# Kernel optimization log

Hardware: AMD Instinct MI355X
Metric: run time of the kernel (lower is better)

The kernel has to match this reference:

```python
import jax, jax.numpy as jnp
import numpy as np


def setup_inputs() -> dict:
    key = jax.random.key(0)
    ks = jax.random.split(key, 6)
    B, C, S, E = 8, 16, 512, 256
    wscale = (2.0 / (E + E)) ** 0.5  # xavier_normal for [E, E] fan_in=fan_out=E
    return {
        "query": jax.random.normal(ks[0], (B, C, S, E), dtype=jnp.float32),
        "key": jax.random.normal(ks[1], (B, C, S, E), dtype=jnp.float32),
        "value": jax.random.normal(ks[2], (B, C, S, E), dtype=jnp.float32),
        "q_proj_weight": jax.random.normal(ks[3], (C, E, E), dtype=jnp.float32) * wscale,
        "k_proj_weight": jax.random.normal(ks[4], (C, E, E), dtype=jnp.float32) * wscale,
        "v_proj_weight": jax.random.normal(ks[5], (C, E, E), dtype=jnp.float32) * wscale,
        "q_proj_bias": jnp.zeros((C, 1, E), dtype=jnp.float32),
        "k_proj_bias": jnp.zeros((C, 1, E), dtype=jnp.float32),
        "v_proj_bias": jnp.zeros((C, 1, E), dtype=jnp.float32),
    }


def reference(query, key, value, q_proj_weight, k_proj_weight, v_proj_weight,
              q_proj_bias, k_proj_bias, v_proj_bias):
    E = query.shape[-1]
    # Per-cycle projection + bias + ReLU.  b=batch, c=cycle, s/t=seq, e/f=embed
    q = jax.nn.relu(jnp.einsum("bcse,cef->bcsf", query, q_proj_weight) + q_proj_bias)
    k = jax.nn.relu(jnp.einsum("bcse,cef->bcsf", key, k_proj_weight) + k_proj_bias)
    v = jax.nn.relu(jnp.einsum("bcse,cef->bcsf", value, v_proj_weight) + v_proj_bias)
    q = q * (float(E) ** -0.5)
    attn = jax.nn.softmax(jnp.einsum("bcse,bcte->bcst", q, k), axis=-1)
    out = jnp.einsum("bcst,bcte->bcse", attn, v)
    return out
```

## Files before the change

### kernel.cpp

```cpp
#include <hip/hip_runtime.h>

constexpr int BATCH = 8;
constexpr int CYC   = 16;
constexpr int SEQ   = 512;
constexpr int EMB   = 256;

typedef __attribute__((ext_vector_type(8))) short bf16x8;
typedef __attribute__((ext_vector_type(4))) float f32x4;

__device__ __forceinline__ unsigned short f2bf(float x) {
    unsigned int u = __float_as_uint(x);
    u += 0x7fffu + ((u >> 16) & 1u);
    return (unsigned short)(u >> 16);
}
__device__ __forceinline__ unsigned int pk2(float lo, float hi) {
    return (unsigned int)f2bf(lo) | ((unsigned int)f2bf(hi) << 16);
}

__device__ __forceinline__ f32x4 mfma16(bf16x8 a, bf16x8 b, f32x4 c) {
    return __builtin_amdgcn_mfma_f32_16x16x32_bf16(a, b, c, 0, 0, 0);
}

__device__ __forceinline__ void gll16(const unsigned short* g, unsigned short* l) {
    __builtin_amdgcn_global_load_lds(
        (const __attribute__((address_space(1))) void*)g,
        (__attribute__((address_space(3))) void*)l, 16, 0, 0);
}

__global__ __launch_bounds__(256) void wt_kernel(const float* __restrict__ W,
                                                 unsigned short* __restrict__ Wt) {
    __shared__ float tile[64][65];
    const int c  = blockIdx.z;
    const int e0 = blockIdx.x * 64;
    const int f0 = blockIdx.y * 64;
    const float* Wc = W + (size_t)c * EMB * EMB;
    unsigned short* Wtc = Wt + (size_t)c * EMB * EMB;
    const int t = threadIdx.x;
    {
        const int er = t >> 4;
        const int fc = (t & 15) * 4;
        for (int i = 0; i < 4; ++i) {
            const float4 v = *(const float4*)(Wc + (size_t)(e0 + er + i * 16) * EMB + f0 + fc);
            tile[er + i * 16][fc + 0] = v.x;
            tile[er + i * 16][fc + 1] = v.y;
            tile[er + i * 16][fc + 2] = v.z;
            tile[er + i * 16][fc + 3] = v.w;
        }
    }
    __syncthreads();
    {
        const int fr = t >> 4;
        const int ec = (t & 15) * 4;
        for (int i = 0; i < 4; ++i) {
            const int f = fr + i * 16;
            ushort4 o;
            o.x = f2bf(tile[ec + 0][f]);
            o.y = f2bf(tile[ec + 1][f]);
            o.z = f2bf(tile[ec + 2][f]);
            o.w = f2bf(tile[ec + 3][f]);
            *(ushort4*)(Wtc + (size_t)(f0 + f) * EMB + e0 + ec) = o;
        }
    }
}

__global__ __launch_bounds__(256) void proj_kernel(
    const float* __restrict__ X, const unsigned short* __restrict__ Wt,
    const float* __restrict__ bias, unsigned short* __restrict__ Y,
    const float scale, const int transposeOut)
{
    __shared__ unsigned short smem[10752];
    unsigned short* As = smem;
    unsigned short* Bs = smem + 2560;
    const int bc = blockIdx.x;
    const int c  = bc & (CYC - 1);
    const int m0 = blockIdx.y * 64;
    const float* Xb = X + (size_t)bc * SEQ * EMB;
    const unsigned short* Wc = Wt + (size_t)c * EMB * EMB;
    const float* bb = bias + (size_t)c * EMB;
    unsigned short* Yb = Y + (size_t)bc * SEQ * EMB;

    const int tid  = threadIdx.x;
    const int lane = tid & 63, w = tid >> 6;
    const int ln   = lane & 15, quad = lane >> 4;
    const int wu   = __builtin_amdgcn_readfirstlane(w);

    const int arow = tid >> 2;
    const int acol = (tid & 3) * 8;
    const int brow = lane >> 2;
    const int gch  = (lane & 3) ^ ((lane >> 3) & 3);
    const int bslot = quad ^ ((ln >> 1) & 3);

    f32x4 acc[4][4];
    for (int i = 0; i < 4; ++i)
        for (int j = 0; j < 4; ++j) acc[i][j] = (f32x4){0.f, 0.f, 0.f, 0.f};

    for (int kk = 0; kk < 8; ++kk) {
        const int k0 = kk * 32;
        const float* ax = Xb + (size_t)(m0 + arow) * EMB + k0 + acol;
        const float4 a0 = *(const float4*)ax;
        const float4 a1 = *(const float4*)(ax + 4);
        int4 pk;
        pk.x = pk2(a0.x, a0.y); pk.y = pk2(a0.z, a0.w);
        pk.z = pk2(a1.x, a1.y); pk.w = pk2(a1.z, a1.w);
        *(int4*)&As[arow * 40 + acol] = pk;
        for (int j = 0; j < 4; ++j) {
            const int r = wu * 64 + j * 16 + brow;
            gll16(Wc + (size_t)r * EMB + k0 + gch * 8,
                  Bs + (size_t)(wu * 64 + j * 16) * 32);
        }
        __syncthreads();
        bf16x8 af[4], bfv[4];
        for (int i = 0; i < 4; ++i)
            af[i] = *(const bf16x8*)&As[(i * 16 + ln) * 40 + quad * 8];
        for (int j = 0; j < 4; ++j)
            bfv[j] = *(const bf16x8*)&Bs[(w * 64 + j * 16 + ln) * 32 + bslot * 8];
        for (int i = 0; i < 4; ++i)
            for (int j = 0; j < 4; ++j)
                acc[i][j] = mfma16(af[i], bfv[j], acc[i][j]);
        __syncthreads();
    }

    float bvj[4];
    for (int j = 0; j < 4; ++j) bvj[j] = bb[w * 64 + j * 16 + ln];

    if (!transposeOut) {
        unsigned short* ep = smem + w * 1152;
        for (int i = 0; i < 4; ++i) {
            for (int j = 0; j < 4; ++j)
                for (int r = 0; r < 4; ++r)
                    ep[(quad * 4 + r) * 72 + j * 16 + ln] =
                        f2bf(fmaxf(acc[i][j][r] + bvj[j], 0.f) * scale);
            __syncthreads();
            for (int h = 0; h < 2; ++h) {
                const int cid = lane + h * 64;
                const int row = cid >> 3, ch = cid & 7;
                *(bf16x8*)&Yb[(size_t)(m0 + i * 16 + row) * EMB + w * 64 + ch * 8] =
                    *(const bf16x8*)&ep[row * 72 + ch * 8];
            }
            __syncthreads();
        }
    } else {
        for (int j = 0; j < 4; ++j) {
            const int fg = w * 64 + j * 16 + ln;
            for (int i = 0; i < 4; ++i) {
                const int mb = m0 + i * 16 + quad * 4;
                ushort4 u;
                u.x = f2bf(fmaxf(acc[i][j][0] + bvj[j], 0.f) * scale);
                u.y = f2bf(fmaxf(acc[i][j][1] + bvj[j], 0.f) * scale);
                u.z = f2bf(fmaxf(acc[i][j][2] + bvj[j], 0.f) * scale);
                u.w = f2bf(fmaxf(acc[i][j][3] + bvj[j], 0.f) * scale);
                *(ushort4*)&Yb[(size_t)fg * SEQ + mb] = u;
            }
        }
    }
}

__global__ __launch_bounds__(256) void attn_kernel(
    const unsigned short* __restrict__ Qp, const unsigned short* __restrict__ Kp,
    const unsigned short* __restrict__ Vt, float* __restrict__ Out)
{
    __shared__ unsigned short Ks[32][264];
    __shared__ unsigned short Vs[256][40];
    __shared__ unsigned short Ps[64][40];
    const int bc = blockIdx.x;
    const int qt = blockIdx.y;
    const unsigned short* Qb = Qp + (size_t)bc * SEQ * EMB;
    const unsigned short* Kb = Kp + (size_t)bc * SEQ * EMB;
    const unsigned short* Vb = Vt + (size_t)bc * SEQ * EMB;
    float* Ob = Out + (size_t)bc * SEQ * EMB;

    const int tid  = threadIdx.x;
    const int lane = tid & 63, w = tid >> 6;
    const int ln   = lane & 15, quad = lane >> 4;

    bf16x8 qf[8];
    const int qrow = qt * 64 + w * 16 + ln;
    for (int ke = 0; ke < 8; ++ke)
        qf[ke] = *(const bf16x8*)(Qb + (size_t)qrow * EMB + ke * 32 + quad * 8);

    f32x4 of[16];
    for (int n = 0; n < 16; ++n) of[n] = (f32x4){0.f, 0.f, 0.f, 0.f};
    float lsum[4] = {0.f, 0.f, 0.f, 0.f};

    for (int tt = 0; tt < 16; ++tt) {
        const int t0 = tt * 32;
        for (int i = 0; i < 4; ++i) {
            const int idx = tid + i * 256;
            const int r = idx >> 5, c8 = (idx & 31) * 8;
            *(bf16x8*)&Ks[r][c8] = *(const bf16x8*)(Kb + (size_t)(t0 + r) * EMB + c8);
        }
        for (int i = 0; i < 4; ++i) {
            const int idx = tid + i * 256;
            const int e = idx >> 2, c8 = (idx & 3) * 8;
            *(bf16x8*)&Vs[e][c8] = *(const bf16x8*)(Vb + (size_t)e * SEQ + t0 + c8);
        }
        __syncthreads();

        f32x4 sf0 = (f32x4){0.f,0.f,0.f,0.f}, sf1 = (f32x4){0.f,0.f,0.f,0.f};
        for (int ke = 0; ke < 8; ++ke) {
            bf16x8 b0 = *(const bf16x8*)&Ks[ln][ke * 32 + quad * 8];
            bf16x8 b1 = *(const bf16x8*)&Ks[16 + ln][ke * 32 + quad * 8];
            sf0 = mfma16(qf[ke], b0, sf0);
            sf1 = mfma16(qf[ke], b1, sf1);
        }

        float p0[4], p1[4];
        for (int r = 0; r < 4; ++r) {
            p0[r] = __expf(sf0[r]);
            p1[r] = __expf(sf1[r]);
            lsum[r] += p0[r] + p1[r];
        }
        for (int r = 0; r < 4; ++r) {
            Ps[w * 16 + quad * 4 + r][ln]      = f2bf(p0[r]);
            Ps[w * 16 + quad * 4 + r][16 + ln] = f2bf(p1[r]);
        }
        __syncthreads();

        bf16x8 af = *(const bf16x8*)&Ps[w * 16 + ln][quad * 8];
        for (int n = 0; n < 16; ++n) {
            bf16x8 bv = *(const bf16x8*)&Vs[n * 16 + ln][quad * 8];
            of[n] = mfma16(af, bv, of[n]);
        }
        __syncthreads();
    }

    for (int off = 1; off < 16; off <<= 1)
        for (int r = 0; r < 4; ++r)
            lsum[r] += __shfl_xor(lsum[r], off, 64);
    float inv[4];
    for (int r = 0; r < 4; ++r) inv[r] = 1.0f / lsum[r];
    const int mbase = qt * 64 + w * 16 + quad * 4;
    for (int n = 0; n < 16; ++n)
        for (int r = 0; r < 4; ++r)
            Ob[(size_t)(mbase + r) * EMB + n * 16 + ln] = of[n][r] * inv[r];
}

extern "C" void kernel_launch(void* const* d_in, const int* in_sizes, int n_in,
                              void* d_out, int out_size, void* d_ws, size_t ws_size,
                              hipStream_t stream) {
    const float* query = (const float*)d_in[0];
    const float* key_  = (const float*)d_in[1];
    const float* value = (const float*)d_in[2];
    const float* wq = (const float*)d_in[3];
    const float* wk = (const float*)d_in[4];
    const float* wv = (const float*)d_in[5];
    const float* bq = (const float*)d_in[6];
    const float* bk = (const float*)d_in[7];
    const float* bv = (const float*)d_in[8];
    float* out = (float*)d_out;

    char* ws = (char*)d_ws;
    const size_t wsz = (size_t)CYC * EMB * EMB * sizeof(unsigned short);
    const size_t psz = (size_t)BATCH * CYC * SEQ * EMB * sizeof(unsigned short);
    unsigned short* Wtq = (unsigned short*)(ws);
    unsigned short* Wtk = (unsigned short*)(ws + wsz);
    unsigned short* Wtv = (unsigned short*)(ws + 2 * wsz);
    unsigned short* Qp  = (unsigned short*)(ws + 3 * wsz);
    unsigned short* Kp  = (unsigned short*)(ws + 3 * wsz + psz);
    unsigned short* Vtp = (unsigned short*)(ws + 3 * wsz + 2 * psz);

    const dim3 tb(256);
    wt_kernel<<<dim3(4, 4, CYC), tb, 0, stream>>>(wq, Wtq);
    wt_kernel<<<dim3(4, 4, CYC), tb, 0, stream>>>(wk, Wtk);
    wt_kernel<<<dim3(4, 4, CYC), tb, 0, stream>>>(wv, Wtv);

    const dim3 pg(BATCH * CYC, SEQ / 64);
    proj_kernel<<<pg, tb, 0, stream>>>(query, Wtq, bq, Qp, 0.0625f, 0);
    proj_kernel<<<pg, tb, 0, stream>>>(key_,  Wtk, bk, Kp, 1.0f, 0);
    proj_kernel<<<pg, tb, 0, stream>>>(value, Wtv, bv, Vtp, 1.0f, 1);

    attn_kernel<<<dim3(BATCH * CYC, SEQ / 64), tb, 0, stream>>>(Qp, Kp, Vtp, out);
}
```

Baseline: 352.4 us.

## Merge launches, pre-swizzle weights, double-buffer proj and attention K tiles

Combines the three weight-transpose launches and the three projection launches into one launch each, selecting Q/K/V by blockIdx.z. The weight-transpose kernel now writes the transposed weights in a k-chunked, pre-swizzled layout, so the projection kernel can fetch contiguous 16-byte chunks with global_load_lds into double-buffered LDS, overlapping the next tile's loads with the current MFMAs. The attention kernel double-buffers K tiles in XOR-swizzled LDS and loads V fragments straight from global into registers instead of staging them through LDS. Occupancy hints are added to the launch bounds. The aim is to cut launch overhead and load latency, at the cost of more LDS and registers per block and uncoalesced direct V loads.

```diff
diff --git a/kernel.cpp b/kernel.cpp
--- a/kernel.cpp
+++ b/kernel.cpp
@@ -16,64 +16,76 @@
 __device__ __forceinline__ unsigned int pk2(float lo, float hi) {
     return (unsigned int)f2bf(lo) | ((unsigned int)f2bf(hi) << 16);
 }
-
 __device__ __forceinline__ f32x4 mfma16(bf16x8 a, bf16x8 b, f32x4 c) {
     return __builtin_amdgcn_mfma_f32_16x16x32_bf16(a, b, c, 0, 0, 0);
 }
-
 __device__ __forceinline__ void gll16(const unsigned short* g, unsigned short* l) {
     __builtin_amdgcn_global_load_lds(
         (const __attribute__((address_space(1))) void*)g,
         (__attribute__((address_space(3))) void*)l, 16, 0, 0);
 }
 
-__global__ __launch_bounds__(256) void wt_kernel(const float* __restrict__ W,
-                                                 unsigned short* __restrict__ Wt) {
-    __shared__ float tile[64][65];
-    const int c  = blockIdx.z;
-    const int e0 = blockIdx.x * 64;
+__global__ __launch_bounds__(256) void wt_kernel(
+    const float* __restrict__ Wq, const float* __restrict__ Wk, const float* __restrict__ Wv,
+    unsigned short* __restrict__ Oq, unsigned short* __restrict__ Ok, unsigned short* __restrict__ Ov)
+{
+    __shared__ float tile[32][65];
+    const int kk = blockIdx.x;
     const int f0 = blockIdx.y * 64;
+    const int z  = blockIdx.z;
+    const int which = z >> 4, c = z & 15;
+    const float* W = which == 0 ? Wq : (which == 1 ? Wk : Wv);
+    unsigned short* O = which == 0 ? Oq : (which == 1 ? Ok : Ov);
     const float* Wc = W + (size_t)c * EMB * EMB;
-    unsigned short* Wtc = Wt + (size_t)c * EMB * EMB;
+    unsigned short* Oc = O + (size_t)c * EMB * EMB;
     const int t = threadIdx.x;
     {
-        const int er = t >> 4;
-        const int fc = (t & 15) * 4;
-        for (int i = 0; i < 4; ++i) {
-            const float4 v = *(const float4*)(Wc + (size_t)(e0 + er + i * 16) * EMB + f0 + fc);
-            tile[er + i * 16][fc + 0] = v.x;
-            tile[er + i * 16][fc + 1] = v.y;
-            tile[er + i * 16][fc + 2] = v.z;
-            tile[er + i * 16][fc + 3] = v.w;
-        }
+        const int er = t >> 3, fc = (t & 7) * 8;
+        const float4 v0 = *(const float4*)(Wc + (size_t)(kk * 32 + er) * EMB + f0 + fc);
+        const float4 v1 = *(const float4*)(Wc + (size_t)(kk * 32 + er) * EMB + f0 + fc + 4);
+        tile[er][fc + 0] = v0.x; tile[er][fc + 1] = v0.y;
+        tile[er][fc + 2] = v0.z; tile[er][fc + 3] = v0.w;
+        tile[er][fc + 4] = v1.x; tile[er][fc + 5] = v1.y;
+        tile[er][fc + 6] = v1.z; tile[er][fc + 7] = v1.w;
     }
     __syncthreads();
     {
-        const int fr = t >> 4;
-        const int ec = (t & 15) * 4;
-        for (int i = 0; i < 4; ++i) {
-            const int f = fr + i * 16;
-            ushort4 o;
-            o.x = f2bf(tile[ec + 0][f]);
-            o.y = f2bf(tile[ec + 1][f]);
-            o.z = f2bf(tile[ec + 2][f]);
-            o.w = f2bf(tile[ec + 3][f]);
-            *(ushort4*)(Wtc + (size_t)(f0 + f) * EMB + e0 + ec) = o;
-        }
-    }
-}
-
-__global__ __launch_bounds__(256) void proj_kernel(
-    const float* __restrict__ X, const unsigned short* __restrict__ Wt,
-    const float* __restrict__ bias, unsigned short* __restrict__ Y,
-    const float scale, const int transposeOut)
+        const int fl = t >> 2, s = t & 3;
+        const int f  = f0 + fl;
+        const int e0 = (s ^ ((f >> 1) & 3)) * 8;
+        ushort4 o0, o1;
+        o0.x = f2bf(tile[e0 + 0][fl]); o0.y = f2bf(tile[e0 + 1][fl]);
+        o0.z = f2bf(tile[e0 + 2][fl]); o0.w = f2bf(tile[e0 + 3][fl]);
+        o1.x = f2bf(tile[e0 + 4][fl]); o1.y = f2bf(tile[e0 + 5][fl]);
+        o1.z = f2bf(tile[e0 + 6][fl]); o1.w = f2bf(tile[e0 + 7][fl]);
+        unsigned short* dst = Oc + (size_t)kk * 8192 + (size_t)f * 32 + s * 8;
+        *(ushort4*)dst       = o0;
+        *(ushort4*)(dst + 4) = o1;
+    }
+}
+
+__global__ __launch_bounds__(256, 3) void proj_kernel(
+    const float* __restrict__ Xq, const float* __restrict__ Xk, const float* __restrict__ Xv,
+    const unsigned short* __restrict__ Wq, const unsigned short* __restrict__ Wk,
+    const unsigned short* __restrict__ Wv,
+    const float* __restrict__ bq, const float* __restrict__ bk, const float* __restrict__ bv,
+    unsigned short* __restrict__ Yq, unsigned short* __restrict__ Yk, unsigned short* __restrict__ Yv)
 {
-    __shared__ unsigned short smem[10752];
-    unsigned short* As = smem;
-    unsigned short* Bs = smem + 2560;
+    __shared__ unsigned short smem[21504];
+    unsigned short* Asb[2] = { smem,        smem + 2560 };
+    unsigned short* Bsb[2] = { smem + 5120, smem + 13312 };
+
     const int bc = blockIdx.x;
+    const int m0 = blockIdx.y * 64;
+    const int which = blockIdx.z;
     const int c  = bc & (CYC - 1);
-    const int m0 = blockIdx.y * 64;
+    const float* X = which == 0 ? Xq : (which == 1 ? Xk : Xv);
+    const unsigned short* Wt = which == 0 ? Wq : (which == 1 ? Wk : Wv);
+    const float* bias = which == 0 ? bq : (which == 1 ? bk : bv);
+    unsigned short* Y = which == 0 ? Yq : (which == 1 ? Yk : Yv);
+    const float scale = which == 0 ? 0.0625f : 1.0f;
+    const int transposeOut = (which == 2);
+
     const float* Xb = X + (size_t)bc * SEQ * EMB;
     const unsigned short* Wc = Wt + (size_t)c * EMB * EMB;
     const float* bb = bias + (size_t)c * EMB;
@@ -84,41 +96,55 @@
     const int ln   = lane & 15, quad = lane >> 4;
     const int wu   = __builtin_amdgcn_readfirstlane(w);
 
-    const int arow = tid >> 2;
-    const int acol = (tid & 3) * 8;
-    const int brow = lane >> 2;
-    const int gch  = (lane & 3) ^ ((lane >> 3) & 3);
+    const int arow  = tid >> 2;
+    const int acol  = (tid & 3) * 8;
     const int bslot = quad ^ ((ln >> 1) & 3);
 
     f32x4 acc[4][4];
     for (int i = 0; i < 4; ++i)
         for (int j = 0; j < 4; ++j) acc[i][j] = (f32x4){0.f, 0.f, 0.f, 0.f};
 
-    for (int kk = 0; kk < 8; ++kk) {
-        const int k0 = kk * 32;
-        const float* ax = Xb + (size_t)(m0 + arow) * EMB + k0 + acol;
+    {
+        const unsigned short* gw = Wc + (size_t)(wu * 64) * 32 + lane * 8;
+        unsigned short* lb = Bsb[0] + (wu * 64) * 32;
+        for (int j = 0; j < 4; ++j) gll16(gw + j * 512, lb + j * 512);
+        const float* ax = Xb + (size_t)(m0 + arow) * EMB + acol;
         const float4 a0 = *(const float4*)ax;
         const float4 a1 = *(const float4*)(ax + 4);
         int4 pk;
         pk.x = pk2(a0.x, a0.y); pk.y = pk2(a0.z, a0.w);
         pk.z = pk2(a1.x, a1.y); pk.w = pk2(a1.z, a1.w);
-        *(int4*)&As[arow * 40 + acol] = pk;
-        for (int j = 0; j < 4; ++j) {
-            const int r = wu * 64 + j * 16 + brow;
-            gll16(Wc + (size_t)r * EMB + k0 + gch * 8,
-                  Bs + (size_t)(wu * 64 + j * 16) * 32);
-        }
+        *(int4*)&Asb[0][arow * 40 + acol] = pk;
+    }
+
+    for (int kk = 0; kk < 8; ++kk) {
+        const int cur = kk & 1, nxt = cur ^ 1;
         __syncthreads();
+        float4 a0n, a1n;
+        if (kk < 7) {
+            const float* ax = Xb + (size_t)(m0 + arow) * EMB + (kk + 1) * 32 + acol;
+            a0n = *(const float4*)ax;
+            a1n = *(const float4*)(ax + 4);
+            const unsigned short* gw = Wc + (size_t)(kk + 1) * 8192 + (wu * 64) * 32 + lane * 8;
+            unsigned short* lb = Bsb[nxt] + (wu * 64) * 32;
+            for (int j = 0; j < 4; ++j) gll16(gw + j * 512, lb + j * 512);
+        }
         bf16x8 af[4], bfv[4];
         for (int i = 0; i < 4; ++i)
-            af[i] = *(const bf16x8*)&As[(i * 16 + ln) * 40 + quad * 8];
+            af[i] = *(const bf16x8*)&Asb[cur][(i * 16 + ln) * 40 + quad * 8];
         for (int j = 0; j < 4; ++j)
-            bfv[j] = *(const bf16x8*)&Bs[(w * 64 + j * 16 + ln) * 32 + bslot * 8];
+            bfv[j] = *(const bf16x8*)&Bsb[cur][(w * 64 + j * 16 + ln) * 32 + bslot * 8];
         for (int i = 0; i < 4; ++i)
             for (int j = 0; j < 4; ++j)
                 acc[i][j] = mfma16(af[i], bfv[j], acc[i][j]);
-        __syncthreads();
-    }
+        if (kk < 7) {
+            int4 pk;
+            pk.x = pk2(a0n.x, a0n.y); pk.y = pk2(a0n.z, a0n.w);
+            pk.z = pk2(a1n.x, a1n.y); pk.w = pk2(a1n.z, a1n.w);
+            *(int4*)&Asb[nxt][arow * 40 + acol] = pk;
+        }
+    }
+    __syncthreads();
 
     float bvj[4];
     for (int j = 0; j < 4; ++j) bvj[j] = bb[w * 64 + j * 16 + ln];
@@ -155,13 +181,12 @@
     }
 }
 
-__global__ __launch_bounds__(256) void attn_kernel(
+__global__ __launch_bounds__(256, 3) void attn_kernel(
     const unsigned short* __restrict__ Qp, const unsigned short* __restrict__ Kp,
     const unsigned short* __restrict__ Vt, float* __restrict__ Out)
 {
-    __shared__ unsigned short Ks[32][264];
-    __shared__ unsigned short Vs[256][40];
-    __shared__ unsigned short Ps[64][40];
+    __shared__ unsigned short Ks[2][8192];
+    __shared__ unsigned short Ps[2560];
     const int bc = blockIdx.x;
     const int qt = blockIdx.y;
     const unsigned short* Qb = Qp + (size_t)bc * SEQ * EMB;
@@ -172,6 +197,7 @@
     const int tid  = threadIdx.x;
     const int lane = tid & 63, w = tid >> 6;
     const int ln   = lane & 15, quad = lane >> 4;
+    const int wu   = __builtin_amdgcn_readfirstlane(w);
 
     bf16x8 qf[8];
     const int qrow = qt * 64 + w * 16 + ln;
@@ -182,24 +208,40 @@
     for (int n = 0; n < 16; ++n) of[n] = (f32x4){0.f, 0.f, 0.f, 0.f};
     float lsum[4] = {0.f, 0.f, 0.f, 0.f};
 
+    const int krow = wu * 8 + (lane >> 5);
+    const int kch  = lane & 31;
+    const size_t voff = (size_t)ln * SEQ + quad * 8;
+
+    {
+        unsigned short* lb = Ks[0] + (wu * 8) * 256;
+        for (int j = 0; j < 4; ++j) {
+            const int row = krow + j * 2;
+            const int gc  = kch ^ (row & 7);
+            gll16(Kb + (size_t)row * EMB + gc * 8, lb + j * 512);
+        }
+    }
+
     for (int tt = 0; tt < 16; ++tt) {
-        const int t0 = tt * 32;
-        for (int i = 0; i < 4; ++i) {
-            const int idx = tid + i * 256;
-            const int r = idx >> 5, c8 = (idx & 31) * 8;
-            *(bf16x8*)&Ks[r][c8] = *(const bf16x8*)(Kb + (size_t)(t0 + r) * EMB + c8);
-        }
-        for (int i = 0; i < 4; ++i) {
-            const int idx = tid + i * 256;
-            const int e = idx >> 2, c8 = (idx & 3) * 8;
-            *(bf16x8*)&Vs[e][c8] = *(const bf16x8*)(Vb + (size_t)e * SEQ + t0 + c8);
-        }
+        const int cur = tt & 1;
         __syncthreads();
+        if (tt < 15) {
+            const int t1 = (tt + 1) * 32;
+            unsigned short* lb = Ks[cur ^ 1] + (wu * 8) * 256;
+            for (int j = 0; j < 4; ++j) {
+                const int row = krow + j * 2;
+                const int gc  = kch ^ (row & 7);
+                gll16(Kb + (size_t)(t1 + row) * EMB + gc * 8, lb + j * 512);
+            }
+        }
+        bf16x8 vf[8];
+        for (int n = 0; n < 8; ++n)
+            vf[n] = *(const bf16x8*)(Vb + voff + (size_t)n * 16 * SEQ + tt * 32);
 
         f32x4 sf0 = (f32x4){0.f,0.f,0.f,0.f}, sf1 = (f32x4){0.f,0.f,0.f,0.f};
         for (int ke = 0; ke < 8; ++ke) {
-            bf16x8 b0 = *(const bf16x8*)&Ks[ln][ke * 32 + quad * 8];
-            bf16x8 b1 = *(const bf16x8*)&Ks[16 + ln][ke * 32 + quad * 8];
+            const int slot = ((ke * 4 + quad) ^ (ln & 7)) * 8;
+            bf16x8 b0 = *(const bf16x8*)&Ks[cur][ln * 256 + slot];
+            bf16x8 b1 = *(const bf16x8*)&Ks[cur][(16 + ln) * 256 + slot];
             sf0 = mfma16(qf[ke], b0, sf0);
             sf1 = mfma16(qf[ke], b1, sf1);
         }
@@ -211,17 +253,19 @@
             lsum[r] += p0[r] + p1[r];
         }
         for (int r = 0; r < 4; ++r) {
-            Ps[w * 16 + quad * 4 + r][ln]      = f2bf(p0[r]);
-            Ps[w * 16 + quad * 4 + r][16 + ln] = f2bf(p1[r]);
+            Ps[(w * 16 + quad * 4 + r) * 40 + ln]      = f2bf(p0[r]);
+            Ps[(w * 16 + quad * 4 + r) * 40 + 16 + ln] = f2bf(p1[r]);
         }
         __syncthreads();
 
-        bf16x8 af = *(const bf16x8*)&Ps[w * 16 + ln][quad * 8];
-        for (int n = 0; n < 16; ++n) {
-            bf16x8 bv = *(const bf16x8*)&Vs[n * 16 + ln][quad * 8];
-            of[n] = mfma16(af, bv, of[n]);
-        }
-        __syncthreads();
+        bf16x8 af = *(const bf16x8*)&Ps[(w * 16 + ln) * 40 + quad * 8];
+        for (int n = 0; n < 8; ++n)
+            of[n] = mfma16(af, vf[n], of[n]);
+        bf16x8 vg[8];
+        for (int n = 0; n < 8; ++n)
+            vg[n] = *(const bf16x8*)(Vb + voff + (size_t)(n + 8) * 16 * SEQ + tt * 32);
+        for (int n = 0; n < 8; ++n)
+            of[n + 8] = mfma16(af, vg[n], of[n + 8]);
     }
 
     for (int off = 1; off < 16; off <<= 1)
@@ -260,14 +304,8 @@
     unsigned short* Vtp = (unsigned short*)(ws + 3 * wsz + 2 * psz);
 
     const dim3 tb(256);
-    wt_kernel<<<dim3(4, 4, CYC), tb, 0, stream>>>(wq, Wtq);
-    wt_kernel<<<dim3(4, 4, CYC), tb, 0, stream>>>(wk, Wtk);
-    wt_kernel<<<dim3(4, 4, CYC), tb, 0, stream>>>(wv, Wtv);
-
-    const dim3 pg(BATCH * CYC, SEQ / 64);
-    proj_kernel<<<pg, tb, 0, stream>>>(query, Wtq, bq, Qp, 0.0625f, 0);
-    proj_kernel<<<pg, tb, 0, stream>>>(key_,  Wtk, bk, Kp, 1.0f, 0);
-    proj_kernel<<<pg, tb, 0, stream>>>(value, Wtv, bv, Vtp, 1.0f, 1);
-
+    wt_kernel<<<dim3(8, 4, 48), tb, 0, stream>>>(wq, wk, wv, Wtq, Wtk, Wtv);
+    proj_kernel<<<dim3(BATCH * CYC, SEQ / 64, 3), tb, 0, stream>>>(
+        query, key_, value, Wtq, Wtk, Wtv, bq, bk, bv, Qp, Kp, Vtp);
     attn_kernel<<<dim3(BATCH * CYC, SEQ / 64), tb, 0, stream>>>(Qp, Kp, Vtp, out);
 }
```

Result: slower. 415.4 us (+17.9%).
